# Kernel optimization log

Hardware: AMD Instinct MI355X
Metric: run time of the kernel (lower is better)

## Reference

```python
import jax, jax.numpy as jnp
import numpy as np


def setup_inputs() -> dict:
    key = jax.random.key(0)
    k1, k2, k3, k4 = jax.random.split(key, 4)
    n, d, h, w = 16, 512, 64, 64
    m, kcodes = 4, 256
    dm = d // m  # 128
    latent = jax.random.normal(k1, (n, d, h, w), dtype=jnp.float32)
    codebook = jax.random.normal(k2, (m, kcodes, dm), dtype=jnp.float32)
    wq = jax.random.normal(k3, (m, dm, dm), dtype=jnp.float32) / np.sqrt(dm)
    wk = jax.random.normal(k4, (m, dm, dm), dtype=jnp.float32) / np.sqrt(dm)
    return {"latent": latent, "codebook": codebook, "wq": wq, "wk": wk}


def reference(latent, codebook, wq, wk):
    # latent: [n, d, h, w]; codebook: [m, k, dm]; wq/wk: [m, dm, dm]
    n, d, h, w = latent.shape
    m, kcodes, dm = codebook.shape
    # NCHW -> NHWC -> [n, h, w, m, dm]
    q = jnp.transpose(latent, (0, 2, 3, 1)).reshape(n, h, w, m, dm)
    # per-group query projection: q @ wq^T (einsum 'nhwmd,mcd->nhwmc')
    q = jnp.einsum('nhwmd,mcd->nhwmc', q, wq)
    # per-group key projection of codebook: 'mkd,mcd->mkc'
    keys = jnp.einsum('mkd,mcd->mkc', codebook, wk)
    # dot-product scores over code dim, then argmax -> code indices
    scores = jnp.einsum('nhwmd,mkd->nhwmk', q, keys)
    code = jnp.argmax(scores, axis=-1).astype(jnp.uint8)
    return code
```

## Files before the change

### kernel.cpp

```cpp
#include <hip/hip_runtime.h>


#define MM   4
#define KC   256
#define DM   128
#define HW   4096
#define WW_  64
#define EPS  0.045f
#define WLC  16384
#define RPB  4
#define RSH  136

typedef _Float16 f16x8 __attribute__((ext_vector_type(8)));
typedef _Float16 f16x4 __attribute__((ext_vector_type(4)));
typedef _Float16 f16x2 __attribute__((ext_vector_type(2)));
typedef float    f32x4 __attribute__((ext_vector_type(4)));
typedef float    f32x2 __attribute__((ext_vector_type(2)));

__global__ __launch_bounds__(128) void a_kernel(const float* __restrict__ wk,
                                                const float* __restrict__ wq,
                                                double* __restrict__ A) {
    int me = blockIdx.x;
    int d  = threadIdx.x;
    int m  = me >> 7;
    int e  = me & 127;
    const float* wkm = wk + (size_t)m * DM * DM + e;
    const float* wqm = wq + (size_t)m * DM * DM + d;
    double s0 = 0.0, s1 = 0.0, s2 = 0.0, s3 = 0.0;
#pragma unroll 8
    for (int c = 0; c < DM; c += 4) {
        s0 = fma((double)wkm[(size_t)(c+0) * DM], (double)wqm[(size_t)(c+0) * DM], s0);
        s1 = fma((double)wkm[(size_t)(c+1) * DM], (double)wqm[(size_t)(c+1) * DM], s1);
        s2 = fma((double)wkm[(size_t)(c+2) * DM], (double)wqm[(size_t)(c+2) * DM], s2);
        s3 = fma((double)wkm[(size_t)(c+3) * DM], (double)wqm[(size_t)(c+3) * DM], s3);
    }
    A[(size_t)me * DM + d] = (s0 + s1) + (s2 + s3);
}

__global__ __launch_bounds__(128) void keff_kernel(const float* __restrict__ cb,
                                                   const double* __restrict__ A,
                                                   double* __restrict__ keffdT,
                                                   _Float16* __restrict__ keff16) {
    int mk = blockIdx.x;
    int d  = threadIdx.x;
    int m  = mk >> 8;
    int k  = mk & 255;
    const float*  cbr = cb + (size_t)mk * DM;
    const double* Am  = A + (size_t)m * DM * DM + d;
    double s0 = 0.0, s1 = 0.0, s2 = 0.0, s3 = 0.0;
#pragma unroll 8
    for (int e = 0; e < DM; e += 4) {
        s0 = fma((double)cbr[e+0], Am[(size_t)(e+0) * DM], s0);
        s1 = fma((double)cbr[e+1], Am[(size_t)(e+1) * DM], s1);
        s2 = fma((double)cbr[e+2], Am[(size_t)(e+2) * DM], s2);
        s3 = fma((double)cbr[e+3], Am[(size_t)(e+3) * DM], s3);
    }
    double s = (s0 + s1) + (s2 + s3);
    keffdT[((size_t)m * DM + d) * KC + k] = s;
    keff16[(size_t)mk * DM + d] = (_Float16)s;
}

__global__ __launch_bounds__(512, 4) void argmax_mfma(const float* __restrict__ latent,
                                                      const _Float16* __restrict__ keff16,
                                                      int* __restrict__ out,
                                                      int* __restrict__ wl_cnt,
                                                      int* __restrict__ wl) {
    __shared__ _Float16 lq[2][64 * RSH];
    __shared__ float pbv[2][64][8];
    __shared__ float psv[2][64][8];
    __shared__ int   pbi[2][64][8];

    int blk  = blockIdx.x;
    int n    = blk >> 5;
    int m    = (blk >> 3) & 3;
    int hg   = blk & 7;
    int tid  = threadIdx.x;
    int wave = tid >> 6;
    int lane = tid & 63;
    int col  = lane & 15;
    int quad = lane >> 4;
    int w2   = (tid & 31) * 2;
    int db   = (tid >> 5) * 8;

    f16x8 Af[2][4];
    {
        const _Float16* kbase = keff16 + ((size_t)m * KC + wave * 32) * DM;
#pragma unroll
        for (int t = 0; t < 2; ++t)
#pragma unroll
            for (int s = 0; s < 4; ++s)
                Af[t][s] = *(const f16x8*)(kbase + (size_t)(t * 16 + col) * DM + s * 32 + quad * 8);
    }

    const float* lp0 = latent + ((size_t)(n * 512 + m * DM)) * HW + (size_t)(hg * 8) * WW_;

    {
        f32x2 pf[8];
#pragma unroll
        for (int pp = 0; pp < 8; ++pp)
            pf[pp] = *(const f32x2*)(lp0 + (size_t)(db + pp) * HW + w2);
#pragma unroll
        for (int j = 0; j < 2; ++j) {
            f16x8 v;
#pragma unroll
            for (int pp = 0; pp < 8; ++pp) v[pp] = (_Float16)pf[pp][j];
            *(f16x8*)&lq[0][(size_t)(w2 + j) * RSH + db] = v;
        }
    }
    __syncthreads();

    for (int r = 0; r < 8; ++r) {
        int cur = r & 1;

        f32x2 pf[8];
        if (r < 7) {
            const float* lp = lp0 + (size_t)(r + 1) * WW_;
#pragma unroll
            for (int pp = 0; pp < 8; ++pp)
                pf[pp] = *(const f32x2*)(lp + (size_t)(db + pp) * HW + w2);
        }

#pragma unroll
        for (int p = 0; p < 4; ++p) {
            f16x8 Bf[4];
#pragma unroll
            for (int s = 0; s < 4; ++s)
                Bf[s] = *(const f16x8*)&lq[cur][(size_t)(p * 16 + col) * RSH + s * 32 + quad * 8];
            f32x4 acc[2];
#pragma unroll
            for (int t = 0; t < 2; ++t) {
                f32x4 c = (f32x4){0.f, 0.f, 0.f, 0.f};
                c = __builtin_amdgcn_mfma_f32_16x16x32_f16(Af[t][0], Bf[0], c, 0, 0, 0);
                c = __builtin_amdgcn_mfma_f32_16x16x32_f16(Af[t][1], Bf[1], c, 0, 0, 0);
                c = __builtin_amdgcn_mfma_f32_16x16x32_f16(Af[t][2], Bf[2], c, 0, 0, 0);
                c = __builtin_amdgcn_mfma_f32_16x16x32_f16(Af[t][3], Bf[3], c, 0, 0, 0);
                acc[t] = c;
            }
            float bv = acc[0][0];
            int   bi = wave * 32 + quad * 4;
            float sv = -3.0e38f;
#pragma unroll
            for (int t = 0; t < 2; ++t)
#pragma unroll
                for (int g = 0; g < 4; ++g) {
                    if (t == 0 && g == 0) continue;
                    float v   = acc[t][g];
                    int   idx = wave * 32 + t * 16 + quad * 4 + g;
                    if (v > bv)      { sv = bv; bv = v; bi = idx; }
                    else if (v > sv) sv = v;
                }
#pragma unroll
            for (int off = 16; off < 64; off <<= 1) {
                float ov = __shfl_xor(bv, off);
                int   oi = __shfl_xor(bi, off);
                float os = __shfl_xor(sv, off);
                bool  take  = (ov > bv) || (ov == bv && oi < bi);
                float loser = take ? bv : ov;
                sv = fmaxf(fmaxf(sv, os), loser);
                if (take) { bv = ov; bi = oi; }
            }
            if (quad == 0) {
                int P = p * 16 + col;
                pbv[cur][P][wave] = bv; psv[cur][P][wave] = sv; pbi[cur][P][wave] = bi;
            }
        }

        if (r < 7) {
#pragma unroll
            for (int j = 0; j < 2; ++j) {
                f16x8 v;
#pragma unroll
                for (int pp = 0; pp < 8; ++pp) v[pp] = (_Float16)pf[pp][j];
                *(f16x8*)&lq[cur ^ 1][(size_t)(w2 + j) * RSH + db] = v;
            }
        }
        __syncthreads();

        {
            int P    = tid >> 3;
            int slot = tid & 7;
            float bv = pbv[cur][P][slot];
            float sv = psv[cur][P][slot];
            int   bi = pbi[cur][P][slot];
#pragma unroll
            for (int off = 1; off < 8; off <<= 1) {
                float ov = __shfl_xor(bv, off);
                int   oi = __shfl_xor(bi, off);
                float os = __shfl_xor(sv, off);
                bool  take  = (ov > bv) || (ov == bv && oi < bi);
                float loser = take ? bv : ov;
                sv = fmaxf(fmaxf(sv, os), loser);
                if (take) { bv = ov; bi = oi; }
            }
            if (slot == 0) {
                int h   = hg * 8 + r;
                int pix = (((n * 64 + h) * 64) + P) * MM + m;
                out[pix] = bi;
                if (bv - sv < EPS) {
                    int s_ = atomicAdd(wl_cnt + m * 16, 1);
                    if (s_ < WLC) wl[m * WLC + s_] = pix;
                }
            }
        }
    }
}

__global__ __launch_bounds__(256) void rescue_kernel(const float* __restrict__ latent,
                                                     const double* __restrict__ keffdT,
                                                     const int* __restrict__ wl_cnt,
                                                     const int* __restrict__ wl,
                                                     int* __restrict__ out) {
    __shared__ double sq[RPB][DM];
    __shared__ double sval[256][RPB];
    __shared__ int    sidx[256][RPB];
    __shared__ int    spix[RPB];
    int b   = blockIdx.x;
    int m   = b & 3;
    int t   = threadIdx.x;
    int cnt = wl_cnt[m * 16];
    if (cnt > WLC) cnt = WLC;
    const int*    wlm = wl + m * WLC;
    const double* krm = keffdT + (size_t)m * DM * KC + t;

    for (int i0 = (b >> 2) * RPB; i0 < cnt; i0 += 256 * RPB) {
        int pi  = t >> 6;
        int dd  = (t & 63) * 2;
        int idx = i0 + pi;
        int vld = idx < cnt;
        int pix = wlm[vld ? idx : i0];
        int rem = pix >> 2;
        int w   = rem & 63;
        int bh  = rem >> 6;
        int n   = bh >> 6;
        int h   = bh & 63;
        const float* lp = latent + ((size_t)(n * 512 + m * DM)) * HW + h * WW_ + w;
        sq[pi][dd]     = (double)lp[(size_t)dd * HW];
        sq[pi][dd + 1] = (double)lp[(size_t)(dd + 1) * HW];
        if ((t & 63) == 0) spix[pi] = vld ? pix : -1;
        __syncthreads();

        double s0 = 0.0, s1 = 0.0, s2 = 0.0, s3 = 0.0;
#pragma unroll 4
        for (int d = 0; d < DM; ++d) {
            double kd = krm[(size_t)d * KC];
            s0 = fma(sq[0][d], kd, s0);
            s1 = fma(sq[1][d], kd, s1);
            s2 = fma(sq[2][d], kd, s2);
            s3 = fma(sq[3][d], kd, s3);
        }
        sval[t][0] = s0; sval[t][1] = s1; sval[t][2] = s2; sval[t][3] = s3;
        sidx[t][0] = t;  sidx[t][1] = t;  sidx[t][2] = t;  sidx[t][3] = t;
        __syncthreads();

        for (int stp = 128; stp > 0; stp >>= 1) {
            if (t < stp) {
#pragma unroll
                for (int p = 0; p < RPB; ++p) {
                    double vo = sval[t + stp][p], vm = sval[t][p];
                    int io = sidx[t + stp][p], im = sidx[t][p];
                    if (vo > vm || (vo == vm && io < im)) { sval[t][p] = vo; sidx[t][p] = io; }
                }
            }
            __syncthreads();
        }
        if (t < RPB) {
            int opix = spix[t];
            if (opix >= 0) out[opix] = sidx[0][t];
        }
        __syncthreads();
    }
}

extern "C" void kernel_launch(void* const* d_in, const int* in_sizes, int n_in,
                              void* d_out, int out_size, void* d_ws, size_t ws_size,
                              hipStream_t stream) {
    const float* latent = (const float*)d_in[0];
    const float* cb     = (const float*)d_in[1];
    const float* wq     = (const float*)d_in[2];
    const float* wk     = (const float*)d_in[3];
    int* out = (int*)d_out;

    char* ws = (char*)d_ws;
    double*   A      = (double*)ws;     ws += (size_t)MM * DM * DM * sizeof(double);
    double*   keffdT = (double*)ws;     ws += (size_t)MM * DM * KC * sizeof(double);
    _Float16* keff16 = (_Float16*)ws;   ws += (size_t)MM * KC * DM * sizeof(_Float16);
    int*      wl_cnt = (int*)ws;        ws += 256;
    int*      wl     = (int*)ws;

    hipMemsetAsync(wl_cnt, 0, 256, stream);
    a_kernel<<<MM * DM, 128, 0, stream>>>(wk, wq, A);
    keff_kernel<<<MM * KC, 128, 0, stream>>>(cb, A, keffdT, keff16);
    argmax_mfma<<<512, 512, 0, stream>>>(latent, keff16, out, wl_cnt, wl);
    rescue_kernel<<<1024, 256, 0, stream>>>(latent, keffdT, wl_cnt, wl, out);
}
```

Measured before the change: 253.6 us.

## Deepen latent prefetch to two rows ahead with ping-pong registers

The argmax kernel now prefetches latent rows two iterations ahead using two register buffers (pfA/pfB) and unrolls the row loop by two through a macro. The fp16 conversion of the already-loaded row happens before the MFMA work, while the next-next row's global loads are issued. This is meant to hide global load latency behind a full iteration of compute. In exchange it raises register pressure (16 more f32x2 values live) under launch_bounds(512,4), which could cause spills or lower occupancy.

```diff
diff --git a/kernel.cpp b/kernel.cpp
--- a/kernel.cpp
+++ b/kernel.cpp
@@ -60,6 +60,97 @@
     keff16[(size_t)mk * DM + d] = (_Float16)s;
 }
 
+#define ARG_BODY(R, CUR, PFC, PFN)                                                \
+  do {                                                                            \
+    f16x8 cv0, cv1;                                                               \
+    if ((R) < 7) {                                                                \
+      _Pragma("unroll")                                                           \
+      for (int pp = 0; pp < 8; ++pp) { cv0[pp] = (_Float16)PFC[pp][0];            \
+                                       cv1[pp] = (_Float16)PFC[pp][1]; }          \
+    }                                                                             \
+    if ((R) < 6) {                                                                \
+      const float* lp_ = lp0 + (size_t)((R) + 2) * WW_;                           \
+      _Pragma("unroll")                                                           \
+      for (int pp = 0; pp < 8; ++pp)                                              \
+        PFN[pp] = *(const f32x2*)(lp_ + (size_t)(db + pp) * HW + w2);             \
+    }                                                                             \
+    _Pragma("unroll")                                                             \
+    for (int p = 0; p < 4; ++p) {                                                 \
+      f16x8 Bf[4];                                                                \
+      _Pragma("unroll")                                                           \
+      for (int s = 0; s < 4; ++s)                                                 \
+        Bf[s] = *(const f16x8*)&lq[CUR][(size_t)(p * 16 + col) * RSH + s * 32 + quad * 8]; \
+      f32x4 acc[2];                                                               \
+      _Pragma("unroll")                                                           \
+      for (int t = 0; t < 2; ++t) {                                               \
+        f32x4 c_ = (f32x4){0.f, 0.f, 0.f, 0.f};                                   \
+        c_ = __builtin_amdgcn_mfma_f32_16x16x32_f16(Af[t][0], Bf[0], c_, 0, 0, 0);\
+        c_ = __builtin_amdgcn_mfma_f32_16x16x32_f16(Af[t][1], Bf[1], c_, 0, 0, 0);\
+        c_ = __builtin_amdgcn_mfma_f32_16x16x32_f16(Af[t][2], Bf[2], c_, 0, 0, 0);\
+        c_ = __builtin_amdgcn_mfma_f32_16x16x32_f16(Af[t][3], Bf[3], c_, 0, 0, 0);\
+        acc[t] = c_;                                                              \
+      }                                                                           \
+      float bv = acc[0][0];                                                       \
+      int   bi = wave * 32 + quad * 4;                                            \
+      float sv = -3.0e38f;                                                        \
+      _Pragma("unroll")                                                           \
+      for (int t = 0; t < 2; ++t)                                                 \
+        _Pragma("unroll")                                                         \
+        for (int g = 0; g < 4; ++g) {                                             \
+          if (t == 0 && g == 0) continue;                                         \
+          float v_   = acc[t][g];                                                 \
+          int   idx_ = wave * 32 + t * 16 + quad * 4 + g;                         \
+          if (v_ > bv)      { sv = bv; bv = v_; bi = idx_; }                      \
+          else if (v_ > sv) sv = v_;                                              \
+        }                                                                         \
+      _Pragma("unroll")                                                           \
+      for (int off = 16; off < 64; off <<= 1) {                                   \
+        float ov = __shfl_xor(bv, off);                                           \
+        int   oi = __shfl_xor(bi, off);                                           \
+        float os = __shfl_xor(sv, off);                                           \
+        bool  take  = (ov > bv) || (ov == bv && oi < bi);                         \
+        float loser = take ? bv : ov;                                             \
+        sv = fmaxf(fmaxf(sv, os), loser);                                         \
+        if (take) { bv = ov; bi = oi; }                                           \
+      }                                                                           \
+      if (quad == 0) {                                                            \
+        int P_ = p * 16 + col;                                                    \
+        pbv[CUR][P_][wave] = bv; psv[CUR][P_][wave] = sv; pbi[CUR][P_][wave] = bi;\
+      }                                                                           \
+    }                                                                             \
+    if ((R) < 7) {                                                                \
+      *(f16x8*)&lq[(CUR) ^ 1][(size_t)(w2 + 0) * RSH + db] = cv0;                 \
+      *(f16x8*)&lq[(CUR) ^ 1][(size_t)(w2 + 1) * RSH + db] = cv1;                 \
+    }                                                                             \
+    __syncthreads();                                                              \
+    {                                                                             \
+      int P_    = tid >> 3;                                                       \
+      int slot_ = tid & 7;                                                        \
+      float bv = pbv[CUR][P_][slot_];                                             \
+      float sv = psv[CUR][P_][slot_];                                             \
+      int   bi = pbi[CUR][P_][slot_];                                             \
+      _Pragma("unroll")                                                           \
+      for (int off = 1; off < 8; off <<= 1) {                                     \
+        float ov = __shfl_xor(bv, off);                                           \
+        int   oi = __shfl_xor(bi, off);                                           \
+        float os = __shfl_xor(sv, off);                                           \
+        bool  take  = (ov > bv) || (ov == bv && oi < bi);                         \
+        float loser = take ? bv : ov;                                             \
+        sv = fmaxf(fmaxf(sv, os), loser);                                         \
+        if (take) { bv = ov; bi = oi; }                                           \
+      }                                                                           \
+      if (slot_ == 0) {                                                           \
+        int h_   = hg * 8 + (R);                                                  \
+        int pix_ = (((n * 64 + h_) * 64) + P_) * MM + m;                          \
+        out[pix_] = bi;                                                           \
+        if (bv - sv < EPS) {                                                      \
+          int s_ = atomicAdd(wl_cnt + m * 16, 1);                                 \
+          if (s_ < WLC) wl[m * WLC + s_] = pix_;                                  \
+        }                                                                         \
+      }                                                                           \
+    }                                                                             \
+  } while (0)
+
 __global__ __launch_bounds__(512, 4) void argmax_mfma(const float* __restrict__ latent,
                                                       const _Float16* __restrict__ keff16,
                                                       int* __restrict__ out,
@@ -94,114 +185,32 @@
 
     const float* lp0 = latent + ((size_t)(n * 512 + m * DM)) * HW + (size_t)(hg * 8) * WW_;
 
+    f32x2 pfA[8], pfB[8];
     {
-        f32x2 pf[8];
+        f32x2 p0[8];
 #pragma unroll
         for (int pp = 0; pp < 8; ++pp)
-            pf[pp] = *(const f32x2*)(lp0 + (size_t)(db + pp) * HW + w2);
+            p0[pp] = *(const f32x2*)(lp0 + (size_t)(db + pp) * HW + w2);
 #pragma unroll
         for (int j = 0; j < 2; ++j) {
             f16x8 v;
 #pragma unroll
-            for (int pp = 0; pp < 8; ++pp) v[pp] = (_Float16)pf[pp][j];
+            for (int pp = 0; pp < 8; ++pp) v[pp] = (_Float16)p0[pp][j];
             *(f16x8*)&lq[0][(size_t)(w2 + j) * RSH + db] = v;
         }
     }
+    {
+        const float* lp_ = lp0 + (size_t)1 * WW_;
+#pragma unroll
+        for (int pp = 0; pp < 8; ++pp)
+            pfA[pp] = *(const f32x2*)(lp_ + (size_t)(db + pp) * HW + w2);
+    }
     __syncthreads();
 
-    for (int r = 0; r < 8; ++r) {
-        int cur = r & 1;
-
-        f32x2 pf[8];
-        if (r < 7) {
-            const float* lp = lp0 + (size_t)(r + 1) * WW_;
-#pragma unroll
-            for (int pp = 0; pp < 8; ++pp)
-                pf[pp] = *(const f32x2*)(lp + (size_t)(db + pp) * HW + w2);
-        }
-
-#pragma unroll
-        for (int p = 0; p < 4; ++p) {
-            f16x8 Bf[4];
-#pragma unroll
-            for (int s = 0; s < 4; ++s)
-                Bf[s] = *(const f16x8*)&lq[cur][(size_t)(p * 16 + col) * RSH + s * 32 + quad * 8];
-            f32x4 acc[2];
-#pragma unroll
-            for (int t = 0; t < 2; ++t) {
-                f32x4 c = (f32x4){0.f, 0.f, 0.f, 0.f};
-                c = __builtin_amdgcn_mfma_f32_16x16x32_f16(Af[t][0], Bf[0], c, 0, 0, 0);
-                c = __builtin_amdgcn_mfma_f32_16x16x32_f16(Af[t][1], Bf[1], c, 0, 0, 0);
-                c = __builtin_amdgcn_mfma_f32_16x16x32_f16(Af[t][2], Bf[2], c, 0, 0, 0);
-                c = __builtin_amdgcn_mfma_f32_16x16x32_f16(Af[t][3], Bf[3], c, 0, 0, 0);
-                acc[t] = c;
-            }
-            float bv = acc[0][0];
-            int   bi = wave * 32 + quad * 4;
-            float sv = -3.0e38f;
-#pragma unroll
-            for (int t = 0; t < 2; ++t)
-#pragma unroll
-                for (int g = 0; g < 4; ++g) {
-                    if (t == 0 && g == 0) continue;
-                    float v   = acc[t][g];
-                    int   idx = wave * 32 + t * 16 + quad * 4 + g;
-                    if (v > bv)      { sv = bv; bv = v; bi = idx; }
-                    else if (v > sv) sv = v;
-                }
-#pragma unroll
-            for (int off = 16; off < 64; off <<= 1) {
-                float ov = __shfl_xor(bv, off);
-                int   oi = __shfl_xor(bi, off);
-                float os = __shfl_xor(sv, off);
-                bool  take  = (ov > bv) || (ov == bv && oi < bi);
-                float loser = take ? bv : ov;
-                sv = fmaxf(fmaxf(sv, os), loser);
-                if (take) { bv = ov; bi = oi; }
-            }
-            if (quad == 0) {
-                int P = p * 16 + col;
-                pbv[cur][P][wave] = bv; psv[cur][P][wave] = sv; pbi[cur][P][wave] = bi;
-            }
-        }
-
-        if (r < 7) {
-#pragma unroll
-            for (int j = 0; j < 2; ++j) {
-                f16x8 v;
-#pragma unroll
-                for (int pp = 0; pp < 8; ++pp) v[pp] = (_Float16)pf[pp][j];
-                *(f16x8*)&lq[cur ^ 1][(size_t)(w2 + j) * RSH + db] = v;
-            }
-        }
-        __syncthreads();
-
-        {
-            int P    = tid >> 3;
-            int slot = tid & 7;
-            float bv = pbv[cur][P][slot];
-            float sv = psv[cur][P][slot];
-            int   bi = pbi[cur][P][slot];
-#pragma unroll
-            for (int off = 1; off < 8; off <<= 1) {
-                float ov = __shfl_xor(bv, off);
-                int   oi = __shfl_xor(bi, off);
-                float os = __shfl_xor(sv, off);
-                bool  take  = (ov > bv) || (ov == bv && oi < bi);
-                float loser = take ? bv : ov;
-                sv = fmaxf(fmaxf(sv, os), loser);
-                if (take) { bv = ov; bi = oi; }
-            }
-            if (slot == 0) {
-                int h   = hg * 8 + r;
-                int pix = (((n * 64 + h) * 64) + P) * MM + m;
-                out[pix] = bi;
-                if (bv - sv < EPS) {
-                    int s_ = atomicAdd(wl_cnt + m * 16, 1);
-                    if (s_ < WLC) wl[m * WLC + s_] = pix;
-                }
-            }
-        }
+    for (int rr = 0; rr < 4; ++rr) {
+        int r0 = 2 * rr;
+        ARG_BODY(r0,     0, pfA, pfB);
+        ARG_BODY(r0 + 1, 1, pfB, pfA);
     }
 }
 
```

Result: no change. 255.3 us (+0.7%).

## Retile argmax waves to 64 codes x 2 pixel tiles, prefetch two rows ahead

Applied to the files above, without the earlier changes.

Each wave now covers 64 codewords across two pixel tiles instead of 32 codewords across four, so every LDS B-fragment load feeds four MFMAs, halving LDS reads per MFMA. The cross-wave reduction shrinks from 8 slots to 4 and runs in only half the threads. The latent prefetch now runs two rows ahead, with the fp16 conversion and LDS store moved before the compute. The memset is also folded into a_kernel to drop one launch. In exchange, per-thread register use rises (Af doubles to 16 vectors) under launch_bounds(512,4).

```diff
diff --git a/kernel.cpp b/kernel.cpp
--- a/kernel.cpp
+++ b/kernel.cpp
@@ -19,7 +19,9 @@
 
 __global__ __launch_bounds__(128) void a_kernel(const float* __restrict__ wk,
                                                 const float* __restrict__ wq,
-                                                double* __restrict__ A) {
+                                                double* __restrict__ A,
+                                                int* __restrict__ wl_cnt) {
+    if (blockIdx.x == 0 && threadIdx.x < 64) wl_cnt[threadIdx.x] = 0;
     int me = blockIdx.x;
     int d  = threadIdx.x;
     int m  = me >> 7;
@@ -66,9 +68,9 @@
                                                       int* __restrict__ wl_cnt,
                                                       int* __restrict__ wl) {
     __shared__ _Float16 lq[2][64 * RSH];
-    __shared__ float pbv[2][64][8];
-    __shared__ float psv[2][64][8];
-    __shared__ int   pbi[2][64][8];
+    __shared__ float pbv[2][64][4];
+    __shared__ float psv[2][64][4];
+    __shared__ int   pbi[2][64][4];
 
     int blk  = blockIdx.x;
     int n    = blk >> 5;
@@ -79,14 +81,16 @@
     int lane = tid & 63;
     int col  = lane & 15;
     int quad = lane >> 4;
+    int cg   = wave >> 1;
+    int ph   = wave & 1;
     int w2   = (tid & 31) * 2;
     int db   = (tid >> 5) * 8;
 
-    f16x8 Af[2][4];
+    f16x8 Af[4][4];
     {
-        const _Float16* kbase = keff16 + ((size_t)m * KC + wave * 32) * DM;
-#pragma unroll
-        for (int t = 0; t < 2; ++t)
+        const _Float16* kbase = keff16 + ((size_t)m * KC + cg * 64) * DM;
+#pragma unroll
+        for (int t = 0; t < 4; ++t)
 #pragma unroll
             for (int s = 0; s < 4; ++s)
                 Af[t][s] = *(const f16x8*)(kbase + (size_t)(t * 16 + col) * DM + s * 32 + quad * 8);
@@ -94,58 +98,70 @@
 
     const float* lp0 = latent + ((size_t)(n * 512 + m * DM)) * HW + (size_t)(hg * 8) * WW_;
 
+    f32x2 pf[8];
     {
-        f32x2 pf[8];
+        f32x2 p0[8];
 #pragma unroll
         for (int pp = 0; pp < 8; ++pp)
-            pf[pp] = *(const f32x2*)(lp0 + (size_t)(db + pp) * HW + w2);
+            p0[pp] = *(const f32x2*)(lp0 + (size_t)(db + pp) * HW + w2);
 #pragma unroll
         for (int j = 0; j < 2; ++j) {
             f16x8 v;
 #pragma unroll
-            for (int pp = 0; pp < 8; ++pp) v[pp] = (_Float16)pf[pp][j];
+            for (int pp = 0; pp < 8; ++pp) v[pp] = (_Float16)p0[pp][j];
             *(f16x8*)&lq[0][(size_t)(w2 + j) * RSH + db] = v;
         }
+    }
+    {
+        const float* lp_ = lp0 + (size_t)1 * WW_;
+#pragma unroll
+        for (int pp = 0; pp < 8; ++pp)
+            pf[pp] = *(const f32x2*)(lp_ + (size_t)(db + pp) * HW + w2);
     }
     __syncthreads();
 
     for (int r = 0; r < 8; ++r) {
         int cur = r & 1;
 
-        f32x2 pf[8];
         if (r < 7) {
-            const float* lp = lp0 + (size_t)(r + 1) * WW_;
+            f16x8 cv0, cv1;
+#pragma unroll
+            for (int pp = 0; pp < 8; ++pp) { cv0[pp] = (_Float16)pf[pp][0];
+                                             cv1[pp] = (_Float16)pf[pp][1]; }
+            *(f16x8*)&lq[cur ^ 1][(size_t)(w2 + 0) * RSH + db] = cv0;
+            *(f16x8*)&lq[cur ^ 1][(size_t)(w2 + 1) * RSH + db] = cv1;
+        }
+        if (r < 6) {
+            const float* lp_ = lp0 + (size_t)(r + 2) * WW_;
 #pragma unroll
             for (int pp = 0; pp < 8; ++pp)
-                pf[pp] = *(const f32x2*)(lp + (size_t)(db + pp) * HW + w2);
-        }
-
-#pragma unroll
-        for (int p = 0; p < 4; ++p) {
-            f16x8 Bf[4];
-#pragma unroll
-            for (int s = 0; s < 4; ++s)
-                Bf[s] = *(const f16x8*)&lq[cur][(size_t)(p * 16 + col) * RSH + s * 32 + quad * 8];
-            f32x4 acc[2];
-#pragma unroll
-            for (int t = 0; t < 2; ++t) {
-                f32x4 c = (f32x4){0.f, 0.f, 0.f, 0.f};
-                c = __builtin_amdgcn_mfma_f32_16x16x32_f16(Af[t][0], Bf[0], c, 0, 0, 0);
-                c = __builtin_amdgcn_mfma_f32_16x16x32_f16(Af[t][1], Bf[1], c, 0, 0, 0);
-                c = __builtin_amdgcn_mfma_f32_16x16x32_f16(Af[t][2], Bf[2], c, 0, 0, 0);
-                c = __builtin_amdgcn_mfma_f32_16x16x32_f16(Af[t][3], Bf[3], c, 0, 0, 0);
-                acc[t] = c;
+                pf[pp] = *(const f32x2*)(lp_ + (size_t)(db + pp) * HW + w2);
+        }
+
+#pragma unroll
+        for (int pl = 0; pl < 2; ++pl) {
+            int p = ph * 2 + pl;
+            f32x4 acc[4];
+#pragma unroll
+            for (int t = 0; t < 4; ++t) acc[t] = (f32x4){0.f, 0.f, 0.f, 0.f};
+#pragma unroll
+            for (int s = 0; s < 4; ++s) {
+                f16x8 Bf = *(const f16x8*)&lq[cur][(size_t)(p * 16 + col) * RSH + s * 32 + quad * 8];
+                acc[0] = __builtin_amdgcn_mfma_f32_16x16x32_f16(Af[0][s], Bf, acc[0], 0, 0, 0);
+                acc[1] = __builtin_amdgcn_mfma_f32_16x16x32_f16(Af[1][s], Bf, acc[1], 0, 0, 0);
+                acc[2] = __builtin_amdgcn_mfma_f32_16x16x32_f16(Af[2][s], Bf, acc[2], 0, 0, 0);
+                acc[3] = __builtin_amdgcn_mfma_f32_16x16x32_f16(Af[3][s], Bf, acc[3], 0, 0, 0);
             }
             float bv = acc[0][0];
-            int   bi = wave * 32 + quad * 4;
+            int   bi = cg * 64 + quad * 4;
             float sv = -3.0e38f;
 #pragma unroll
-            for (int t = 0; t < 2; ++t)
+            for (int t = 0; t < 4; ++t)
 #pragma unroll
                 for (int g = 0; g < 4; ++g) {
                     if (t == 0 && g == 0) continue;
                     float v   = acc[t][g];
-                    int   idx = wave * 32 + t * 16 + quad * 4 + g;
+                    int   idx = cg * 64 + t * 16 + quad * 4 + g;
                     if (v > bv)      { sv = bv; bv = v; bi = idx; }
                     else if (v > sv) sv = v;
                 }
@@ -161,29 +177,19 @@
             }
             if (quad == 0) {
                 int P = p * 16 + col;
-                pbv[cur][P][wave] = bv; psv[cur][P][wave] = sv; pbi[cur][P][wave] = bi;
-            }
-        }
-
-        if (r < 7) {
-#pragma unroll
-            for (int j = 0; j < 2; ++j) {
-                f16x8 v;
-#pragma unroll
-                for (int pp = 0; pp < 8; ++pp) v[pp] = (_Float16)pf[pp][j];
-                *(f16x8*)&lq[cur ^ 1][(size_t)(w2 + j) * RSH + db] = v;
+                pbv[cur][P][cg] = bv; psv[cur][P][cg] = sv; pbi[cur][P][cg] = bi;
             }
         }
         __syncthreads();
 
-        {
-            int P    = tid >> 3;
-            int slot = tid & 7;
+        if (tid < 256) {
+            int P    = tid >> 2;
+            int slot = tid & 3;
             float bv = pbv[cur][P][slot];
             float sv = psv[cur][P][slot];
             int   bi = pbi[cur][P][slot];
 #pragma unroll
-            for (int off = 1; off < 8; off <<= 1) {
+            for (int off = 1; off < 4; off <<= 1) {
                 float ov = __shfl_xor(bv, off);
                 int   oi = __shfl_xor(bi, off);
                 float os = __shfl_xor(sv, off);
@@ -287,8 +293,7 @@
     int*      wl_cnt = (int*)ws;        ws += 256;
     int*      wl     = (int*)ws;
 
-    hipMemsetAsync(wl_cnt, 0, 256, stream);
-    a_kernel<<<MM * DM, 128, 0, stream>>>(wk, wq, A);
+    a_kernel<<<MM * DM, 128, 0, stream>>>(wk, wq, A, wl_cnt);
     keff_kernel<<<MM * KC, 128, 0, stream>>>(cb, A, keffdT, keff16);
     argmax_mfma<<<512, 512, 0, stream>>>(latent, keff16, out, wl_cnt, wl);
     rescue_kernel<<<1024, 256, 0, stream>>>(latent, keffdT, wl_cnt, wl, out);
```

Measured after the change: 279.6 us. 1.1x slower.

## Fuse key projection setup and rescue pass into fewer kernels

Applied to the files above, without the earlier changes.

The A-matrix and keff kernels are merged into one setup kernel that computes each effective key as wq·(wk·codebook row) through a shared-memory intermediate, so the separate A buffer is no longer needed. The fp64 rescue pass for near-tie pixels moves into the tail of the argmax kernel, using a per-block shared worklist instead of a global atomic worklist plus a separate launch. This removes the memset, two launches and the global atomics. In exchange, blocks that hit many near-ties run a serial fp64 tail that can unbalance load, and shared-memory use per block goes up, which may lower occupancy.

```diff
diff --git a/kernel.cpp b/kernel.cpp
--- a/kernel.cpp
+++ b/kernel.cpp
@@ -7,68 +7,68 @@
 #define HW   4096
 #define WW_  64
 #define EPS  0.045f
-#define WLC  16384
-#define RPB  4
 #define RSH  136
 
 typedef _Float16 f16x8 __attribute__((ext_vector_type(8)));
 typedef _Float16 f16x4 __attribute__((ext_vector_type(4)));
-typedef _Float16 f16x2 __attribute__((ext_vector_type(2)));
 typedef float    f32x4 __attribute__((ext_vector_type(4)));
 typedef float    f32x2 __attribute__((ext_vector_type(2)));
 
-__global__ __launch_bounds__(128) void a_kernel(const float* __restrict__ wk,
-                                                const float* __restrict__ wq,
-                                                double* __restrict__ A) {
-    int me = blockIdx.x;
-    int d  = threadIdx.x;
-    int m  = me >> 7;
-    int e  = me & 127;
-    const float* wkm = wk + (size_t)m * DM * DM + e;
-    const float* wqm = wq + (size_t)m * DM * DM + d;
-    double s0 = 0.0, s1 = 0.0, s2 = 0.0, s3 = 0.0;
+__global__ __launch_bounds__(128) void setup_kernel(const float* __restrict__ cb,
+                                                    const float* __restrict__ wk,
+                                                    const float* __restrict__ wq,
+                                                    double* __restrict__ keffdT,
+                                                    _Float16* __restrict__ keff16) {
+    __shared__ double cbs[DM];
+    __shared__ double u[DM];
+    int mk = blockIdx.x;
+    int m  = mk >> 8;
+    int t  = threadIdx.x;
+    cbs[t] = (double)cb[(size_t)mk * DM + t];
+    __syncthreads();
+    {
+        const f32x4* wkr = (const f32x4*)(wk + (size_t)m * DM * DM + (size_t)t * DM);
+        double s0 = 0.0, s1 = 0.0, s2 = 0.0, s3 = 0.0;
 #pragma unroll 8
-    for (int c = 0; c < DM; c += 4) {
-        s0 = fma((double)wkm[(size_t)(c+0) * DM], (double)wqm[(size_t)(c+0) * DM], s0);
-        s1 = fma((double)wkm[(size_t)(c+1) * DM], (double)wqm[(size_t)(c+1) * DM], s1);
-        s2 = fma((double)wkm[(size_t)(c+2) * DM], (double)wqm[(size_t)(c+2) * DM], s2);
-        s3 = fma((double)wkm[(size_t)(c+3) * DM], (double)wqm[(size_t)(c+3) * DM], s3);
-    }
-    A[(size_t)me * DM + d] = (s0 + s1) + (s2 + s3);
-}
-
-__global__ __launch_bounds__(128) void keff_kernel(const float* __restrict__ cb,
-                                                   const double* __restrict__ A,
-                                                   double* __restrict__ keffdT,
-                                                   _Float16* __restrict__ keff16) {
-    int mk = blockIdx.x;
-    int d  = threadIdx.x;
-    int m  = mk >> 8;
-    int k  = mk & 255;
-    const float*  cbr = cb + (size_t)mk * DM;
-    const double* Am  = A + (size_t)m * DM * DM + d;
-    double s0 = 0.0, s1 = 0.0, s2 = 0.0, s3 = 0.0;
+        for (int e4 = 0; e4 < DM / 4; ++e4) {
+            f32x4 v = wkr[e4];
+            s0 = fma(cbs[4 * e4 + 0], (double)v[0], s0);
+            s1 = fma(cbs[4 * e4 + 1], (double)v[1], s1);
+            s2 = fma(cbs[4 * e4 + 2], (double)v[2], s2);
+            s3 = fma(cbs[4 * e4 + 3], (double)v[3], s3);
+        }
+        u[t] = (s0 + s1) + (s2 + s3);
+    }
+    __syncthreads();
+    {
+        const float* wqc = wq + (size_t)m * DM * DM + t;
+        double s0 = 0.0, s1 = 0.0, s2 = 0.0, s3 = 0.0;
 #pragma unroll 8
-    for (int e = 0; e < DM; e += 4) {
-        s0 = fma((double)cbr[e+0], Am[(size_t)(e+0) * DM], s0);
-        s1 = fma((double)cbr[e+1], Am[(size_t)(e+1) * DM], s1);
-        s2 = fma((double)cbr[e+2], Am[(size_t)(e+2) * DM], s2);
-        s3 = fma((double)cbr[e+3], Am[(size_t)(e+3) * DM], s3);
-    }
-    double s = (s0 + s1) + (s2 + s3);
-    keffdT[((size_t)m * DM + d) * KC + k] = s;
-    keff16[(size_t)mk * DM + d] = (_Float16)s;
+        for (int c = 0; c < DM; c += 4) {
+            s0 = fma(u[c+0], (double)wqc[(size_t)(c+0) * DM], s0);
+            s1 = fma(u[c+1], (double)wqc[(size_t)(c+1) * DM], s1);
+            s2 = fma(u[c+2], (double)wqc[(size_t)(c+2) * DM], s2);
+            s3 = fma(u[c+3], (double)wqc[(size_t)(c+3) * DM], s3);
+        }
+        double s = (s0 + s1) + (s2 + s3);
+        keffdT[((size_t)m * DM + t) * KC + (mk & 255)] = s;
+        keff16[(size_t)mk * DM + t] = (_Float16)s;
+    }
 }
 
 __global__ __launch_bounds__(512, 4) void argmax_mfma(const float* __restrict__ latent,
                                                       const _Float16* __restrict__ keff16,
-                                                      int* __restrict__ out,
-                                                      int* __restrict__ wl_cnt,
-                                                      int* __restrict__ wl) {
+                                                      const double* __restrict__ keffdT,
+                                                      int* __restrict__ out) {
     __shared__ _Float16 lq[2][64 * RSH];
     __shared__ float pbv[2][64][8];
     __shared__ float psv[2][64][8];
     __shared__ int   pbi[2][64][8];
+    __shared__ int   wlb[512];
+    __shared__ int   lcnt;
+    __shared__ double sq[8][DM];
+    __shared__ double rbv[8][4];
+    __shared__ int    rbi[8][4];
 
     int blk  = blockIdx.x;
     int n    = blk >> 5;
@@ -94,6 +94,7 @@
 
     const float* lp0 = latent + ((size_t)(n * 512 + m * DM)) * HW + (size_t)(hg * 8) * WW_;
 
+    if (tid == 0) lcnt = 0;
     {
         f32x2 pf[8];
 #pragma unroll
@@ -197,75 +198,76 @@
                 int pix = (((n * 64 + h) * 64) + P) * MM + m;
                 out[pix] = bi;
                 if (bv - sv < EPS) {
-                    int s_ = atomicAdd(wl_cnt + m * 16, 1);
-                    if (s_ < WLC) wl[m * WLC + s_] = pix;
+                    int s_ = atomicAdd(&lcnt, 1);
+                    wlb[s_] = pix;
                 }
             }
         }
     }
-}
-
-__global__ __launch_bounds__(256) void rescue_kernel(const float* __restrict__ latent,
-                                                     const double* __restrict__ keffdT,
-                                                     const int* __restrict__ wl_cnt,
-                                                     const int* __restrict__ wl,
-                                                     int* __restrict__ out) {
-    __shared__ double sq[RPB][DM];
-    __shared__ double sval[256][RPB];
-    __shared__ int    sidx[256][RPB];
-    __shared__ int    spix[RPB];
-    int b   = blockIdx.x;
-    int m   = b & 3;
-    int t   = threadIdx.x;
-    int cnt = wl_cnt[m * 16];
-    if (cnt > WLC) cnt = WLC;
-    const int*    wlm = wl + m * WLC;
-    const double* krm = keffdT + (size_t)m * DM * KC + t;
-
-    for (int i0 = (b >> 2) * RPB; i0 < cnt; i0 += 256 * RPB) {
-        int pi  = t >> 6;
-        int dd  = (t & 63) * 2;
-        int idx = i0 + pi;
-        int vld = idx < cnt;
-        int pix = wlm[vld ? idx : i0];
-        int rem = pix >> 2;
-        int w   = rem & 63;
-        int bh  = rem >> 6;
-        int n   = bh >> 6;
-        int h   = bh & 63;
-        const float* lp = latent + ((size_t)(n * 512 + m * DM)) * HW + h * WW_ + w;
-        sq[pi][dd]     = (double)lp[(size_t)dd * HW];
-        sq[pi][dd + 1] = (double)lp[(size_t)(dd + 1) * HW];
-        if ((t & 63) == 0) spix[pi] = vld ? pix : -1;
-        __syncthreads();
-
-        double s0 = 0.0, s1 = 0.0, s2 = 0.0, s3 = 0.0;
+
+    __syncthreads();
+    int cnt = lcnt;
+    int pg  = tid >> 8;
+    int kk  = tid & 255;
+    for (int base = 0; base < cnt; base += 8) {
+        {
+            int pi  = tid >> 6;
+            int dd  = (tid & 63) * 2;
+            int idx = base + pi;
+            int pix = wlb[idx < cnt ? idx : base];
+            int rem = pix >> 2;
+            int w   = rem & 63;
+            int bh  = rem >> 6;
+            int nn  = bh >> 6;
+            int hh  = bh & 63;
+            const float* lp = latent + ((size_t)(nn * 512 + m * DM)) * HW + hh * WW_ + w;
+            sq[pi][dd]     = (double)lp[(size_t)dd * HW];
+            sq[pi][dd + 1] = (double)lp[(size_t)(dd + 1) * HW];
+        }
+        __syncthreads();
+        const double* kr = keffdT + (size_t)m * DM * KC + kk;
+        const double* q0 = sq[pg * 4 + 0];
+        const double* q1 = sq[pg * 4 + 1];
+        const double* q2 = sq[pg * 4 + 2];
+        const double* q3 = sq[pg * 4 + 3];
+        double a0 = 0.0, a1 = 0.0, a2 = 0.0, a3 = 0.0;
 #pragma unroll 4
         for (int d = 0; d < DM; ++d) {
-            double kd = krm[(size_t)d * KC];
-            s0 = fma(sq[0][d], kd, s0);
-            s1 = fma(sq[1][d], kd, s1);
-            s2 = fma(sq[2][d], kd, s2);
-            s3 = fma(sq[3][d], kd, s3);
-        }
-        sval[t][0] = s0; sval[t][1] = s1; sval[t][2] = s2; sval[t][3] = s3;
-        sidx[t][0] = t;  sidx[t][1] = t;  sidx[t][2] = t;  sidx[t][3] = t;
-        __syncthreads();
-
-        for (int stp = 128; stp > 0; stp >>= 1) {
-            if (t < stp) {
-#pragma unroll
-                for (int p = 0; p < RPB; ++p) {
-                    double vo = sval[t + stp][p], vm = sval[t][p];
-                    int io = sidx[t + stp][p], im = sidx[t][p];
-                    if (vo > vm || (vo == vm && io < im)) { sval[t][p] = vo; sidx[t][p] = io; }
-                }
-            }
-            __syncthreads();
-        }
-        if (t < RPB) {
-            int opix = spix[t];
-            if (opix >= 0) out[opix] = sidx[0][t];
+            double kd = kr[(size_t)d * KC];
+            a0 = fma(q0[d], kd, a0);
+            a1 = fma(q1[d], kd, a1);
+            a2 = fma(q2[d], kd, a2);
+            a3 = fma(q3[d], kd, a3);
+        }
+        int i0 = kk, i1 = kk, i2 = kk, i3 = kk;
+#pragma unroll
+        for (int off = 1; off < 64; off <<= 1) {
+            double o0 = __shfl_xor(a0, off); int j0 = __shfl_xor(i0, off);
+            double o1 = __shfl_xor(a1, off); int j1 = __shfl_xor(i1, off);
+            double o2 = __shfl_xor(a2, off); int j2 = __shfl_xor(i2, off);
+            double o3 = __shfl_xor(a3, off); int j3 = __shfl_xor(i3, off);
+            if (o0 > a0 || (o0 == a0 && j0 < i0)) { a0 = o0; i0 = j0; }
+            if (o1 > a1 || (o1 == a1 && j1 < i1)) { a1 = o1; i1 = j1; }
+            if (o2 > a2 || (o2 == a2 && j2 < i2)) { a2 = o2; i2 = j2; }
+            if (o3 > a3 || (o3 == a3 && j3 < i3)) { a3 = o3; i3 = j3; }
+        }
+        if ((tid & 63) == 0) {
+            int kw = (tid >> 6) & 3;
+            int pb = pg * 4;
+            rbv[pb + 0][kw] = a0; rbi[pb + 0][kw] = i0;
+            rbv[pb + 1][kw] = a1; rbi[pb + 1][kw] = i1;
+            rbv[pb + 2][kw] = a2; rbi[pb + 2][kw] = i2;
+            rbv[pb + 3][kw] = a3; rbi[pb + 3][kw] = i3;
+        }
+        __syncthreads();
+        if (tid < 8 && base + tid < cnt) {
+            double bv = rbv[tid][0]; int bi = rbi[tid][0];
+#pragma unroll
+            for (int kw = 1; kw < 4; ++kw) {
+                double ov = rbv[tid][kw]; int oi = rbi[tid][kw];
+                if (ov > bv || (ov == bv && oi < bi)) { bv = ov; bi = oi; }
+            }
+            out[wlb[base + tid]] = bi;
         }
         __syncthreads();
     }
@@ -281,15 +283,9 @@
     int* out = (int*)d_out;
 
     char* ws = (char*)d_ws;
-    double*   A      = (double*)ws;     ws += (size_t)MM * DM * DM * sizeof(double);
     double*   keffdT = (double*)ws;     ws += (size_t)MM * DM * KC * sizeof(double);
-    _Float16* keff16 = (_Float16*)ws;   ws += (size_t)MM * KC * DM * sizeof(_Float16);
-    int*      wl_cnt = (int*)ws;        ws += 256;
-    int*      wl     = (int*)ws;
-
-    hipMemsetAsync(wl_cnt, 0, 256, stream);
-    a_kernel<<<MM * DM, 128, 0, stream>>>(wk, wq, A);
-    keff_kernel<<<MM * KC, 128, 0, stream>>>(cb, A, keffdT, keff16);
-    argmax_mfma<<<512, 512, 0, stream>>>(latent, keff16, out, wl_cnt, wl);
-    rescue_kernel<<<1024, 256, 0, stream>>>(latent, keffdT, wl_cnt, wl, out);
+    _Float16* keff16 = (_Float16*)ws;
+
+    setup_kernel<<<MM * KC, 128, 0, stream>>>(cb, wk, wq, keffdT, keff16);
+    argmax_mfma<<<512, 512, 0, stream>>>(latent, keff16, keffdT, out);
 }
```

Measured after the change: 250.6 us. About the same (-1.2%).
